# Kernel optimization log

Measured on AMD Instinct MI355X. Metric: run time of the kernel, lower is better.

Reference implementation:

```python
import jax, jax.numpy as jnp
import numpy as np

N, C_IN, C_OUT, T, V = 32, 4, 64, 6, 512


def setup_inputs() -> dict:
    key = jax.random.key(0)
    ks = jax.random.split(key, 8)
    x = jax.random.normal(ks[0], (N, C_IN, T, V), dtype=jnp.float32)
    # A carries 7 (unused) adjacency channels + 1 binary mask channel
    A = jax.random.randint(ks[1], (N, 8, V, V), 0, 2, dtype=jnp.int32)
    conv_w = jax.random.normal(ks[2], (C_OUT, C_IN), dtype=jnp.float32) / np.sqrt(C_IN).astype(np.float32)
    conv_b = jax.random.normal(ks[3], (C_OUT,), dtype=jnp.float32) * 0.02
    l2_w = jax.random.normal(ks[4], (1, T), dtype=jnp.float32) / np.sqrt(T).astype(np.float32)
    l2_b = jax.random.normal(ks[5], (1,), dtype=jnp.float32) * 0.02
    l1_w = jax.random.normal(ks[6], (1, 2 * C_OUT), dtype=jnp.float32) / np.sqrt(2 * C_OUT).astype(np.float32)
    l1_b = jax.random.normal(ks[7], (1,), dtype=jnp.float32) * 0.02
    return {"x": x, "A": A, "conv_w": conv_w, "conv_b": conv_b,
            "l2_w": l2_w, "l2_b": l2_b, "l1_w": l1_w, "l1_b": l1_b}


def reference(x, A, conv_w, conv_b, l2_w, l2_b, l1_w, l1_b):
    c = conv_w.shape[0]
    # 1x1 conv over (t, v): pure channel mix
    xc = jnp.einsum('nctv,oc->notv', x, conv_w) + conv_b[None, :, None, None]  # (n, 64, t, v)
    # temporal squeeze via l2: Linear(6 -> 1) on last (t) axis
    x1 = jnp.einsum('nctv,t->nvc', xc, l2_w[0]) + l2_b[0]  # (n, v, 64)
    # GAT-style pairwise score: l1(cat(x1_i, x1_j)) decomposes into two rank-1 terms
    e_i = x1 @ l1_w[0, :c]   # (n, v)
    e_j = x1 @ l1_w[0, c:]   # (n, v)
    scores = e_i[:, :, None] + e_j[:, None, :] + l1_b[0]  # (n, v, v), [n,i,j]
    scores = jnp.where(scores >= 0, scores, 0.2 * scores)  # LeakyReLU(0.2)
    # mask channel: A[:,7]; mask.long()==0 -> -inf
    mask = A[:, 7]  # (n, v, v) int
    scores = jnp.where(mask == 0, -jnp.inf, scores)
    p = jax.nn.softmax(scores, axis=2)
    p = jnp.where(jnp.isnan(p), 0.0, p)  # fully-masked rows -> 0
    # aggregate: nctv,ndvw->nctw with d=1
    out = jnp.einsum('nctv,nvw->nctw', xc, p)
    return out, p[:, None]  # (n, 64, t, v), (n, 1, v, v)
```

## Files before the change

### kernel.cpp

```cpp
#include <hip/hip_runtime.h>
#include <math.h>

#define NB   32
#define CIN  4
#define COUT 64
#define TT   6
#define VV   512
#define P_OFF (NB*COUT*TT*VV)
#define SPLITS 8
#define CH   (VV/SPLITS)
#define NROW 24
#define E_FLOATS (2*NB*VV)

__global__ __launch_bounds__(256) void e_kernel(
    const float* __restrict__ x,
    const float* __restrict__ conv_w,
    const float* __restrict__ conv_b,
    const float* __restrict__ l2_w,
    const float* __restrict__ l2_b,
    const float* __restrict__ l1_w,
    float* __restrict__ e)
{
    __shared__ float W1[CIN], W2[CIN], cst[2];
    int tid = threadIdx.x;
    if (tid < CIN) {
        float w1 = 0.f, w2 = 0.f;
        for (int o = 0; o < COUT; ++o) {
            w1 += l1_w[o]        * conv_w[o*CIN + tid];
            w2 += l1_w[COUT + o] * conv_w[o*CIN + tid];
        }
        W1[tid] = w1; W2[tid] = w2;
    }
    if (tid == CIN) {
        float B1 = 0.f, B2 = 0.f, S1 = 0.f, S2 = 0.f;
        for (int o = 0; o < COUT; ++o) {
            B1 += l1_w[o]        * conv_b[o];
            B2 += l1_w[COUT + o] * conv_b[o];
            S1 += l1_w[o];
            S2 += l1_w[COUT + o];
        }
        float Ls = 0.f;
        for (int t = 0; t < TT; ++t) Ls += l2_w[t];
        cst[0] = Ls*B1 + l2_b[0]*S1;
        cst[1] = Ls*B2 + l2_b[0]*S2;
    }
    __syncthreads();

    int idx = blockIdx.x * 256 + tid;
    int n = idx >> 9, v = idx & (VV-1);
    float ei = cst[0], ej = cst[1];
    #pragma unroll
    for (int c = 0; c < CIN; ++c) {
        float wc1 = W1[c], wc2 = W2[c];
        #pragma unroll
        for (int t = 0; t < TT; ++t) {
            float xv = x[((n*CIN + c)*TT + t)*VV + v];
            float lw = l2_w[t];
            ei += lw*wc1*xv;
            ej += lw*wc2*xv;
        }
    }
    e[idx]         = ei;
    e[NB*VV + idx] = ej;
}

__global__ __launch_bounds__(512, 2) void fused_kernel(
    const float* __restrict__ x,
    const int*   __restrict__ A,
    const float* __restrict__ e,
    const float* __restrict__ l1_b,
    float*       __restrict__ p,
    float*       __restrict__ ypart)
{
    __shared__ float xst[NROW][CH];
    __shared__ float ps[16][VV];

    int s = blockIdx.x;
    int n = blockIdx.y;
    int tid = threadIdx.x;
    int lane = tid & 63;
    int q = tid >> 6;
    int rg = q >> 1;
    int wh = q & 1;

    for (int l = tid; l < NROW*CH; l += 512) {
        int r = l >> 6, i = l & 63;
        xst[r][i] = x[((size_t)n*NROW + r)*VV + s*CH + i];
    }

    float l1b_val = l1_b[0];
    float4 ej0 = *(const float4*)(e + NB*VV + n*VV + lane*8);
    float4 ej1 = *(const float4*)(e + NB*VV + n*VV + lane*8 + 4);
    float ejv[8] = {ej0.x, ej0.y, ej0.z, ej0.w, ej1.x, ej1.y, ej1.z, ej1.w};

    const int* mbase = A + (size_t)(n*8 + 7)*VV*VV;

    float acc[6][4];
    #pragma unroll
    for (int rr = 0; rr < 6; ++rr)
        #pragma unroll
        for (int k = 0; k < 4; ++k) acc[rr][k] = 0.f;
    float a24[4] = {0.f, 0.f, 0.f, 0.f};

    int iA0 = s*CH + q*2;
    int4 mA0, mA1, mB0, mB1;
    float bA, bB;
    {
        const int* mrA = mbase + (size_t)iA0*VV + lane*8;
        mA0 = *(const int4*)mrA;       mA1 = *(const int4*)(mrA + 4);
        mB0 = *(const int4*)(mrA+VV);  mB1 = *(const int4*)(mrA + VV + 4);
        bA = e[n*VV + iA0]; bB = e[n*VV + iA0 + 1];
    }

    __syncthreads();

    for (int sub = 0; sub < 4; ++sub) {
        int ilA  = sub*16 + q*2;
        int i_gA = s*CH + ilA;

        int4 cA0 = mA0, cA1 = mA1, cB0 = mB0, cB1 = mB1;
        float biasA = bA + l1b_val, biasB = bB + l1b_val;

        if (sub < 3) {
            const int* mrA = mbase + (size_t)(i_gA + 16)*VV + lane*8;
            mA0 = *(const int4*)mrA;       mA1 = *(const int4*)(mrA + 4);
            mB0 = *(const int4*)(mrA+VV);  mB1 = *(const int4*)(mrA + VV + 4);
            bA = e[n*VV + i_gA + 16]; bB = e[n*VV + i_gA + 17];
        }

        float svA[8], svB[8];
        int mkA[8] = {cA0.x,cA0.y,cA0.z,cA0.w, cA1.x,cA1.y,cA1.z,cA1.w};
        int mkB[8] = {cB0.x,cB0.y,cB0.z,cB0.w, cB1.x,cB1.y,cB1.z,cB1.w};
        #pragma unroll
        for (int m2 = 0; m2 < 8; ++m2) {
            float tA = biasA + ejv[m2]; tA = (tA >= 0.f) ? tA : 0.2f*tA;
            svA[m2] = (mkA[m2] == 0) ? -INFINITY : tA;
            float tB = biasB + ejv[m2]; tB = (tB >= 0.f) ? tB : 0.2f*tB;
            svB[m2] = (mkB[m2] == 0) ? -INFINITY : tB;
        }
        float mA = svA[0], mB = svB[0];
        #pragma unroll
        for (int m2 = 1; m2 < 8; ++m2) {
            mA = fmaxf(mA, svA[m2]); mB = fmaxf(mB, svB[m2]);
        }
        #pragma unroll
        for (int off = 32; off; off >>= 1) {
            mA = fmaxf(mA, __shfl_xor(mA, off));
            mB = fmaxf(mB, __shfl_xor(mB, off));
        }
        float sumA = 0.f, sumB = 0.f;
        if (mA > -INFINITY) {
            #pragma unroll
            for (int m2 = 0; m2 < 8; ++m2) { svA[m2] = __expf(svA[m2]-mA); sumA += svA[m2]; }
        } else {
            #pragma unroll
            for (int m2 = 0; m2 < 8; ++m2) svA[m2] = 0.f;
        }
        if (mB > -INFINITY) {
            #pragma unroll
            for (int m2 = 0; m2 < 8; ++m2) { svB[m2] = __expf(svB[m2]-mB); sumB += svB[m2]; }
        } else {
            #pragma unroll
            for (int m2 = 0; m2 < 8; ++m2) svB[m2] = 0.f;
        }
        #pragma unroll
        for (int off = 32; off; off >>= 1) {
            sumA += __shfl_xor(sumA, off);
            sumB += __shfl_xor(sumB, off);
        }
        float invA = (sumA > 0.f) ? 1.f/sumA : 0.f;
        float invB = (sumB > 0.f) ? 1.f/sumB : 0.f;

        float4 pA03 = {svA[0]*invA, svA[1]*invA, svA[2]*invA, svA[3]*invA};
        float4 pA47 = {svA[4]*invA, svA[5]*invA, svA[6]*invA, svA[7]*invA};
        float4 pB03 = {svB[0]*invB, svB[1]*invB, svB[2]*invB, svB[3]*invB};
        float4 pB47 = {svB[4]*invB, svB[5]*invB, svB[6]*invB, svB[7]*invB};

        float* prA = p + ((size_t)(n*VV + i_gA))*VV + lane*8;
        *(float4*)prA        = pA03;
        *(float4*)(prA + 4)  = pA47;
        *(float4*)(prA + VV)     = pB03;
        *(float4*)(prA + VV + 4) = pB47;

        *(float4*)&ps[q*2][lane*8]       = pA03;
        *(float4*)&ps[q*2][lane*8 + 4]   = pA47;
        *(float4*)&ps[q*2+1][lane*8]     = pB03;
        *(float4*)&ps[q*2+1][lane*8 + 4] = pB47;

        __syncthreads();

        #pragma unroll
        for (int i = 0; i < 16; ++i) {
            float pv0 = ps[i][wh*256 + 0*64 + lane];
            float pv1 = ps[i][wh*256 + 1*64 + lane];
            float pv2 = ps[i][wh*256 + 2*64 + lane];
            float pv3 = ps[i][wh*256 + 3*64 + lane];
            #pragma unroll
            for (int rr = 0; rr < 6; ++rr) {
                float xv = xst[rg*6 + rr][sub*16 + i];
                acc[rr][0] = fmaf(xv, pv0, acc[rr][0]);
                acc[rr][1] = fmaf(xv, pv1, acc[rr][1]);
                acc[rr][2] = fmaf(xv, pv2, acc[rr][2]);
                acc[rr][3] = fmaf(xv, pv3, acc[rr][3]);
            }
            a24[0] += pv0; a24[1] += pv1; a24[2] += pv2; a24[3] += pv3;
        }
        __syncthreads();
    }

    float* yo = ypart + (size_t)(s*NB + n)*25*VV + wh*256 + lane;
    #pragma unroll
    for (int rr = 0; rr < 6; ++rr)
        #pragma unroll
        for (int k = 0; k < 4; ++k)
            yo[(size_t)(rg*6 + rr)*VV + k*64] = acc[rr][k];
    if (rg == 0) {
        #pragma unroll
        for (int k = 0; k < 4; ++k)
            yo[(size_t)24*VV + k*64] = a24[k];
    }
}

__global__ __launch_bounds__(256) void expand_kernel(
    const float* __restrict__ ypart,
    const float* __restrict__ conv_w,
    const float* __restrict__ conv_b,
    float*       __restrict__ out)
{
    __shared__ float ysm[25][64];
    __shared__ float wsm[COUT*CIN];
    __shared__ float bsm[COUT];

    int wc = blockIdx.x;
    int n  = blockIdx.y;
    int tid = threadIdx.x;

    if (tid < COUT*CIN) wsm[tid] = conv_w[tid];
    if (tid < COUT)     bsm[tid] = conv_b[tid];

    for (int l4 = tid; l4 < 400; l4 += 256) {
        int r = l4 >> 4, w4 = l4 & 15;
        float4 a = {0.f, 0.f, 0.f, 0.f};
        #pragma unroll
        for (int s = 0; s < SPLITS; ++s) {
            float4 v = *(const float4*)(ypart +
                ((size_t)(s*NB + n)*25 + r)*VV + wc*64 + w4*4);
            a.x += v.x; a.y += v.y; a.z += v.z; a.w += v.w;
        }
        *(float4*)&ysm[r][w4*4] = a;
    }
    __syncthreads();

    int w  = tid & 63;
    int og = tid >> 6;

    float y[25];
    #pragma unroll
    for (int r = 0; r < 25; ++r) y[r] = ysm[r][w];

    #pragma unroll
    for (int oo = 0; oo < 16; ++oo) {
        int o = og*16 + oo;
        float wb[CIN];
        #pragma unroll
        for (int c = 0; c < CIN; ++c) wb[c] = wsm[o*CIN + c];
        float bo = bsm[o];
        #pragma unroll
        for (int t = 0; t < TT; ++t) {
            float val = bo * y[24];
            #pragma unroll
            for (int c = 0; c < CIN; ++c) val = fmaf(wb[c], y[c*TT + t], val);
            out[((size_t)(n*COUT + o)*TT + t)*VV + wc*64 + w] = val;
        }
    }
}

extern "C" void kernel_launch(void* const* d_in, const int* in_sizes, int n_in,
                              void* d_out, int out_size, void* d_ws, size_t ws_size,
                              hipStream_t stream)
{
    const float* x      = (const float*)d_in[0];
    const int*   A      = (const int*)  d_in[1];
    const float* conv_w = (const float*)d_in[2];
    const float* conv_b = (const float*)d_in[3];
    const float* l2_w   = (const float*)d_in[4];
    const float* l2_b   = (const float*)d_in[5];
    const float* l1_w   = (const float*)d_in[6];
    const float* l1_b   = (const float*)d_in[7];

    float* out = (float*)d_out;
    float* pP  = out + P_OFF;
    float* e   = (float*)d_ws;
    float* yp  = e + E_FLOATS;

    e_kernel<<<NB*VV/256, 256, 0, stream>>>(x, conv_w, conv_b, l2_w, l2_b, l1_w, e);

    dim3 gf(SPLITS, NB);
    fused_kernel<<<gf, 512, 0, stream>>>(x, A, e, l1_b, pP, yp);

    dim3 ge(8, NB);
    expand_kernel<<<ge, 256, 0, stream>>>(yp, conv_w, conv_b, out);
}
```

Before: 39.22 us.

## Double-buffer probability tile, vectorize LDS reads and partial-sum stores

```diff
diff --git a/kernel.cpp b/kernel.cpp
--- a/kernel.cpp
+++ b/kernel.cpp
@@ -72,8 +72,8 @@
     float*       __restrict__ p,
     float*       __restrict__ ypart)
 {
-    __shared__ float xst[NROW][CH];
-    __shared__ float ps[16][VV];
+    __shared__ float xst[CH][4][8];
+    __shared__ float ps[2][16][VV];
 
     int s = blockIdx.x;
     int n = blockIdx.y;
@@ -85,7 +85,7 @@
 
     for (int l = tid; l < NROW*CH; l += 512) {
         int r = l >> 6, i = l & 63;
-        xst[r][i] = x[((size_t)n*NROW + r)*VV + s*CH + i];
+        xst[i][r/6][r%6] = x[((size_t)n*NROW + r)*VV + s*CH + i];
     }
 
     float l1b_val = l1_b[0];
@@ -112,11 +112,8 @@
         bA = e[n*VV + iA0]; bB = e[n*VV + iA0 + 1];
     }
 
-    __syncthreads();
-
     for (int sub = 0; sub < 4; ++sub) {
-        int ilA  = sub*16 + q*2;
-        int i_gA = s*CH + ilA;
+        int i_gA = s*CH + sub*16 + q*2;
 
         int4 cA0 = mA0, cA1 = mA1, cB0 = mB0, cB1 = mB1;
         float biasA = bA + l1b_val, biasB = bB + l1b_val;
@@ -177,47 +174,48 @@
         float4 pB47 = {svB[4]*invB, svB[5]*invB, svB[6]*invB, svB[7]*invB};
 
         float* prA = p + ((size_t)(n*VV + i_gA))*VV + lane*8;
-        *(float4*)prA        = pA03;
-        *(float4*)(prA + 4)  = pA47;
+        *(float4*)prA            = pA03;
+        *(float4*)(prA + 4)      = pA47;
         *(float4*)(prA + VV)     = pB03;
         *(float4*)(prA + VV + 4) = pB47;
 
-        *(float4*)&ps[q*2][lane*8]       = pA03;
-        *(float4*)&ps[q*2][lane*8 + 4]   = pA47;
-        *(float4*)&ps[q*2+1][lane*8]     = pB03;
-        *(float4*)&ps[q*2+1][lane*8 + 4] = pB47;
+        float* pd = &ps[sub & 1][q*2][lane*8];
+        *(float4*)pd          = pA03;
+        *(float4*)(pd + 4)    = pA47;
+        *(float4*)(pd + VV)   = pB03;
+        *(float4*)(pd + VV+4) = pB47;
 
         __syncthreads();
 
+        const float (*psb)[VV] = ps[sub & 1];
         #pragma unroll
         for (int i = 0; i < 16; ++i) {
-            float pv0 = ps[i][wh*256 + 0*64 + lane];
-            float pv1 = ps[i][wh*256 + 1*64 + lane];
-            float pv2 = ps[i][wh*256 + 2*64 + lane];
-            float pv3 = ps[i][wh*256 + 3*64 + lane];
-            #pragma unroll
-            for (int rr = 0; rr < 6; ++rr) {
-                float xv = xst[rg*6 + rr][sub*16 + i];
-                acc[rr][0] = fmaf(xv, pv0, acc[rr][0]);
-                acc[rr][1] = fmaf(xv, pv1, acc[rr][1]);
-                acc[rr][2] = fmaf(xv, pv2, acc[rr][2]);
-                acc[rr][3] = fmaf(xv, pv3, acc[rr][3]);
+            float4 pv = *(const float4*)&psb[i][wh*256 + lane*4];
+            float4 xa = *(const float4*)&xst[sub*16 + i][rg][0];
+            float2 xb = *(const float2*)&xst[sub*16 + i][rg][4];
+            float xr[6] = {xa.x, xa.y, xa.z, xa.w, xb.x, xb.y};
+            float pvk[4] = {pv.x, pv.y, pv.z, pv.w};
+            #pragma unroll
+            for (int rr = 0; rr < 6; ++rr)
+                #pragma unroll
+                for (int k = 0; k < 4; ++k)
+                    acc[rr][k] = fmaf(xr[rr], pvk[k], acc[rr][k]);
+            if (rg == 0) {
+                #pragma unroll
+                for (int k = 0; k < 4; ++k) a24[k] += pvk[k];
             }
-            a24[0] += pv0; a24[1] += pv1; a24[2] += pv2; a24[3] += pv3;
-        }
-        __syncthreads();
-    }
-
-    float* yo = ypart + (size_t)(s*NB + n)*25*VV + wh*256 + lane;
-    #pragma unroll
-    for (int rr = 0; rr < 6; ++rr)
-        #pragma unroll
-        for (int k = 0; k < 4; ++k)
-            yo[(size_t)(rg*6 + rr)*VV + k*64] = acc[rr][k];
+        }
+    }
+
+    float* yo = ypart + (size_t)(s*NB + n)*25*VV + wh*256 + lane*4;
+    #pragma unroll
+    for (int rr = 0; rr < 6; ++rr) {
+        float4 st = {acc[rr][0], acc[rr][1], acc[rr][2], acc[rr][3]};
+        *(float4*)(yo + (size_t)(rg*6 + rr)*VV) = st;
+    }
     if (rg == 0) {
-        #pragma unroll
-        for (int k = 0; k < 4; ++k)
-            yo[(size_t)24*VV + k*64] = a24[k];
+        float4 st = {a24[0], a24[1], a24[2], a24[3]};
+        *(float4*)(yo + (size_t)24*VV) = st;
     }
 }
 
```

Measured after the change: 37.96 us. 3.2% less time.
